# Performance work log

Hardware: AMD Instinct MI355X
Metric: run time of the kernel (lower is better)

Reference implementation:

```python
import jax, jax.numpy as jnp
import numpy as np

B, S, D, H, DQ, DV = 4, 1024, 1024, 16, 64, 64
EPS = 1e-5  # torch LayerNorm default


def setup_inputs() -> dict:
    key = jax.random.key(0)
    ks = jax.random.split(key, 6)
    x = jax.random.normal(ks[0], (B, S, D), dtype=jnp.float32)
    scale = 0.02
    return {
        "query_sequences": x,
        "key_sequences": x,   # self-attention: identical tensors
        "value_sequences": x,
        "key_value_sequence_lengths": jax.random.randint(ks[1], (B,), 512, S + 1, dtype=jnp.int32),
        "ln_gamma": jnp.ones((D,), jnp.float32),
        "ln_beta": jnp.zeros((D,), jnp.float32),
        "Wq": scale * jax.random.normal(ks[2], (D, H * DQ), jnp.float32),
        "bq": jnp.zeros((H * DQ,), jnp.float32),
        "Wk": scale * jax.random.normal(ks[3], (D, H * DQ), jnp.float32),
        "bk": jnp.zeros((H * DQ,), jnp.float32),
        "Wv": scale * jax.random.normal(ks[4], (D, H * DV), jnp.float32),
        "bv": jnp.zeros((H * DV,), jnp.float32),
    }


def _layer_norm(x, gamma, beta):
    mu = jnp.mean(x, axis=-1, keepdims=True)
    var = jnp.mean(jnp.square(x - mu), axis=-1, keepdims=True)
    return (x - mu) * jax.lax.rsqrt(var + EPS) * gamma + beta


def reference(query_sequences, key_sequences, value_sequences,
              key_value_sequence_lengths, ln_gamma, ln_beta,
              Wq, bq, Wk, bk, Wv, bv):
    # self-attention path (query/key/value sequences are identical):
    # pre-LayerNorm applied to all three, causal + pad masking, dropout=0.
    x_in = query_sequences
    xn = _layer_norm(x_in, ln_gamma, ln_beta)

    q = (xn @ Wq + bq).reshape(B, S, H, DQ).transpose(0, 2, 1, 3)  # (B,H,S,DQ)
    k = (xn @ Wk + bk).reshape(B, S, H, DQ).transpose(0, 2, 1, 3)
    v = (xn @ Wv + bv).reshape(B, S, H, DV).transpose(0, 2, 1, 3)

    scores = jnp.einsum("bhqd,bhkd->bhqk", q, k) * (1.0 / np.sqrt(DQ))

    kv_pos = jnp.arange(S)
    pad_mask = kv_pos[None, None, None, :] < key_value_sequence_lengths[:, None, None, None]
    causal = jnp.tril(jnp.ones((S, S), dtype=bool))[None, None]
    mask = pad_mask & causal
    scores = jnp.where(mask, scores, -jnp.inf)

    attn = jax.nn.softmax(scores, axis=-1)  # (B,H,S,S)

    out = jnp.einsum("bhqk,bhkd->bhqd", attn, v)          # (B,H,S,DV)
    out = out.transpose(0, 2, 1, 3).reshape(B, S, H * DV)  # (B,S,D)
    # d_model == n_heads*d_values -> cast_output is Identity; residual is plain sum
    seq = x_in + out
    return seq, attn
```

## Files before the change

### kernel.cpp

```cpp
#include <hip/hip_runtime.h>
#include <stdint.h>

#define BB 4
#define SS 1024
#define DD 1024
#define HH 16

typedef __attribute__((ext_vector_type(8))) __bf16 bf16x8;
typedef __attribute__((ext_vector_type(4))) float f32x4;

__device__ __forceinline__ unsigned short f2bf(float f) {
  union { float ff; uint32_t u; } a; a.ff = f;
  uint32_t r = a.u + 0x7fffu + ((a.u >> 16) & 1u);
  return (unsigned short)(r >> 16);
}

__device__ __forceinline__ float bf2f(unsigned short u) {
  union { uint32_t uu; float ff; } a; a.uu = ((uint32_t)u) << 16;
  return a.ff;
}

__device__ __forceinline__ f32x4 mfma16(bf16x8 a, bf16x8 b, f32x4 c) {
  return __builtin_amdgcn_mfma_f32_16x16x32_bf16(a, b, c, 0, 0, 0);
}

__device__ __forceinline__ void async16(const unsigned short* g, unsigned short* l) {
  __builtin_amdgcn_global_load_lds(
      (__attribute__((address_space(1))) void*)(g),
      (__attribute__((address_space(3))) void*)(l), 16u, 0, 0u);
}

__global__ __launch_bounds__(256) void wtrans_kernel(const float* __restrict__ Wq,
                                                     const float* __restrict__ Wk,
                                                     const float* __restrict__ Wv,
                                                     unsigned short* __restrict__ Wtq,
                                                     unsigned short* __restrict__ Wtk,
                                                     unsigned short* __restrict__ Wtv) {
  __shared__ unsigned short t[64][65];
  const int z = blockIdx.z;
  const float* W = (z == 0) ? Wq : (z == 1) ? Wk : Wv;
  unsigned short* Wt = (z == 0) ? Wtq : (z == 1) ? Wtk : Wtv;
  const int k0 = blockIdx.x * 64, n0 = blockIdx.y * 64;
  const int c = threadIdx.x & 63, r0 = threadIdx.x >> 6;
#pragma unroll
  for (int i = 0; i < 16; ++i) {
    int r = i * 4 + r0;
    t[r][c] = f2bf(W[(size_t)(k0 + r) * DD + n0 + c]);
  }
  __syncthreads();
#pragma unroll
  for (int i = 0; i < 16; ++i) {
    int n = i * 4 + r0;
    Wt[(size_t)(n0 + n) * DD + k0 + c] = t[c][n];
  }
}

__global__ __launch_bounds__(256) void ln_kernel(const float* __restrict__ X,
                                                 const float* __restrict__ gamma,
                                                 const float* __restrict__ beta,
                                                 unsigned short* __restrict__ Xn) {
  const int row = blockIdx.x;
  const int tid = threadIdx.x;
  const float* xr = X + (size_t)row * DD;
  float4 v = ((const float4*)xr)[tid];
  float s = v.x + v.y + v.z + v.w;
  float s2 = v.x * v.x + v.y * v.y + v.z * v.z + v.w * v.w;
#pragma unroll
  for (int off = 1; off < 64; off <<= 1) {
    s += __shfl_xor(s, off);
    s2 += __shfl_xor(s2, off);
  }
  __shared__ float red[8];
  const int wv = tid >> 6, lane = tid & 63;
  if (lane == 0) { red[wv] = s; red[4 + wv] = s2; }
  __syncthreads();
  s = red[0] + red[1] + red[2] + red[3];
  s2 = red[4] + red[5] + red[6] + red[7];
  const float mu = s * (1.0f / DD);
  const float rs = rsqrtf(s2 * (1.0f / DD) - mu * mu + 1e-5f);
  float4 g = ((const float4*)gamma)[tid];
  float4 bt = ((const float4*)beta)[tid];
  ushort4 o;
  o.x = f2bf((v.x - mu) * rs * g.x + bt.x);
  o.y = f2bf((v.y - mu) * rs * g.y + bt.y);
  o.z = f2bf((v.z - mu) * rs * g.z + bt.z);
  o.w = f2bf((v.w - mu) * rs * g.w + bt.w);
  ((ushort4*)(Xn + (size_t)row * DD))[tid] = o;
}

__global__ __launch_bounds__(256) void gemm_qkv_kernel(
    const unsigned short* __restrict__ Xn,
    const unsigned short* __restrict__ Wtq, const unsigned short* __restrict__ Wtk,
    const unsigned short* __restrict__ Wtv,
    const float* __restrict__ bq, const float* __restrict__ bk, const float* __restrict__ bv,
    unsigned short* __restrict__ Qb, unsigned short* __restrict__ Kb,
    unsigned short* __restrict__ Vt) {
  __shared__ __align__(16) unsigned short smem[128 * 136];
  unsigned short* sA = smem;
  unsigned short* sB = smem + 128 * 32;
  const int z = blockIdx.z;
  const unsigned short* Wt = (z == 0) ? Wtq : (z == 1) ? Wtk : Wtv;
  const float* bias = (z == 0) ? bq : (z == 1) ? bk : bv;
  const int tid = threadIdx.x;
  const int lane = tid & 63, wv = tid >> 6;
  const int quad = lane >> 4, l16 = lane & 15;
  const int m0 = blockIdx.x * 128, n0 = blockIdx.y * 128;
  const int wm = (wv & 1) * 64, wn = (wv >> 1) * 64;

  f32x4 acc[4][4];
#pragma unroll
  for (int i = 0; i < 4; ++i)
#pragma unroll
    for (int j = 0; j < 4; ++j) acc[i][j] = (f32x4){0.f, 0.f, 0.f, 0.f};

  for (int kt = 0; kt < DD; kt += 32) {
    __syncthreads();
#pragma unroll
    for (int it = 0; it < 2; ++it) {
      const int c = it * 256 + tid;
      const int row = c >> 2, kc = c & 3;
      async16(Xn + (size_t)(m0 + row) * DD + kt + kc * 8, &sA[(it * 256 + wv * 64) * 8]);
      async16(Wt + (size_t)(n0 + row) * DD + kt + kc * 8, &sB[(it * 256 + wv * 64) * 8]);
    }
    __syncthreads();
    bf16x8 af[4], bfr[4];
#pragma unroll
    for (int i = 0; i < 4; ++i) af[i] = *(const bf16x8*)&sA[(wm + i * 16 + l16) * 32 + quad * 8];
#pragma unroll
    for (int j = 0; j < 4; ++j) bfr[j] = *(const bf16x8*)&sB[(wn + j * 16 + l16) * 32 + quad * 8];
#pragma unroll
    for (int i = 0; i < 4; ++i)
#pragma unroll
      for (int j = 0; j < 4; ++j) acc[i][j] = mfma16(af[i], bfr[j], acc[i][j]);
  }

  if (z < 2) {
    __syncthreads();
    unsigned short* sC = smem;
#pragma unroll
    for (int i = 0; i < 4; ++i) {
      const int lr0 = wm + i * 16 + quad * 4;
#pragma unroll
      for (int j = 0; j < 4; ++j) {
        const int lc = wn + j * 16 + l16;
        const float bb = bias[n0 + lc];
#pragma unroll
        for (int r = 0; r < 4; ++r) sC[(lr0 + r) * 136 + lc] = f2bf(acc[i][j][r] + bb);
      }
    }
    __syncthreads();
    unsigned short* Out = (z == 0) ? Qb : Kb;
    const int rr = tid >> 4, c8 = (tid & 15) * 8;
#pragma unroll
    for (int it = 0; it < 8; ++it) {
      const int row = it * 16 + rr;
      *(uint4*)&Out[(size_t)(m0 + row) * DD + n0 + c8] = *(const uint4*)&sC[row * 136 + c8];
    }
  } else {
#pragma unroll
    for (int i = 0; i < 4; ++i) {
      const int gm0 = m0 + wm + i * 16 + quad * 4;
#pragma unroll
      for (int j = 0; j < 4; ++j) {
        const int gn = n0 + wn + j * 16 + l16;
        const float bb = bias[gn];
        const int b = gm0 >> 10, s0 = gm0 & 1023;
        const int h = gn >> 6, dv = gn & 63;
        ushort4 pk;
        pk.x = f2bf(acc[i][j][0] + bb);
        pk.y = f2bf(acc[i][j][1] + bb);
        pk.z = f2bf(acc[i][j][2] + bb);
        pk.w = f2bf(acc[i][j][3] + bb);
        *(ushort4*)&Vt[((size_t)((b * HH + h) * 64 + dv)) * SS + s0] = pk;
      }
    }
  }
}

__global__ __launch_bounds__(256) void attn_kernel(
    const unsigned short* __restrict__ Qb, const unsigned short* __restrict__ Kb,
    const unsigned short* __restrict__ Vt, const float* __restrict__ X,
    const int* __restrict__ lens, float* __restrict__ seq_out,
    float* __restrict__ attn_out) {
  __shared__ unsigned short sQV[128 * 64];
  __shared__ unsigned short sK[128 * 64];
  __shared__ unsigned short sP[4 * 32 * 128];

  const int tid = threadIdx.x;
  const int lane = tid & 63, wv = tid >> 6;
  const int quad = lane >> 4, l16 = lane & 15;
  const int h = blockIdx.y, b = blockIdx.z;
  const int qt = (b & 2) ? (7 - (int)blockIdx.x) : (int)blockIdx.x;
  const int q0 = qt * 128;
  const int len = lens[b];
  const int KE = min(q0 + 128, len);
  const int NKT = (KE + 127) >> 7;
  const float SCL = 0.1803368801111204f;

#pragma unroll
  for (int it = 0; it < 4; ++it) {
    const int c = it * 256 + tid;
    async16(Qb + (size_t)(b * SS + q0 + (c >> 3)) * DD + h * 64 + (c & 7) * 8,
            &sQV[(it * 256 + wv * 64) * 8]);
  }
  __syncthreads();

  bf16x8 qf[2][2];
#pragma unroll
  for (int i = 0; i < 2; ++i)
#pragma unroll
    for (int dd = 0; dd < 2; ++dd)
      qf[i][dd] = *(const bf16x8*)&sQV[(wv * 32 + i * 16 + l16) * 64 + dd * 32 + quad * 8];

  float lsum[2][4];
#pragma unroll
  for (int i = 0; i < 2; ++i)
#pragma unroll
    for (int r = 0; r < 4; ++r) lsum[i][r] = 0.f;

  for (int kt = 0; kt < NKT; ++kt) {
    const int k0 = kt * 128;
    __syncthreads();
#pragma unroll
    for (int it = 0; it < 4; ++it) {
      const int c = it * 256 + tid;
      async16(Kb + (size_t)(b * SS + k0 + (c >> 3)) * DD + h * 64 + (c & 7) * 8,
              &sK[(it * 256 + wv * 64) * 8]);
    }
    __syncthreads();
    const bool edge = (kt == qt) || (k0 + 128 > len);
#pragma unroll
    for (int j = 0; j < 8; ++j) {
      const bf16x8 kf0 = *(const bf16x8*)&sK[(j * 16 + l16) * 64 + quad * 8];
      const bf16x8 kf1 = *(const bf16x8*)&sK[(j * 16 + l16) * 64 + 32 + quad * 8];
      const int k = k0 + j * 16 + l16;
#pragma unroll
      for (int i = 0; i < 2; ++i) {
        f32x4 sc = (f32x4){0.f, 0.f, 0.f, 0.f};
        sc = mfma16(qf[i][0], kf0, sc);
        sc = mfma16(qf[i][1], kf1, sc);
        const int qq = q0 + wv * 32 + i * 16 + quad * 4;
#pragma unroll
        for (int r = 0; r < 4; ++r) {
          float sv = sc[r] * SCL;
          if (edge && ((k > qq + r) || (k >= len))) sv = -1e30f;
          lsum[i][r] += __builtin_amdgcn_exp2f(sv);
        }
      }
    }
  }

  float linv[2][4];
#pragma unroll
  for (int i = 0; i < 2; ++i)
#pragma unroll
    for (int r = 0; r < 4; ++r) {
      float l = lsum[i][r];
      l += __shfl_xor(l, 1);
      l += __shfl_xor(l, 2);
      l += __shfl_xor(l, 4);
      l += __shfl_xor(l, 8);
      linv[i][r] = 1.0f / l;
    }

  f32x4 oacc[2][4];
#pragma unroll
  for (int i = 0; i < 2; ++i)
#pragma unroll
    for (int jv = 0; jv < 4; ++jv) oacc[i][jv] = (f32x4){0.f, 0.f, 0.f, 0.f};

  const size_t abase = (size_t)(b * HH + h) * SS * SS;

  for (int kt = 0; kt < NKT; ++kt) {
    const int k0 = kt * 128;
    __syncthreads();
#pragma unroll
    for (int it = 0; it < 4; ++it) {
      const int c = it * 256 + tid;
      async16(Kb + (size_t)(b * SS + k0 + (c >> 3)) * DD + h * 64 + (c & 7) * 8,
              &sK[(it * 256 + wv * 64) * 8]);
      async16(Vt + ((size_t)((b * HH + h) * 64 + (c >> 4))) * SS + k0 + (c & 15) * 8,
              &sQV[(it * 256 + wv * 64) * 8]);
    }
    __syncthreads();
    const bool edge = (kt == qt) || (k0 + 128 > len);
#pragma unroll
    for (int j = 0; j < 8; ++j) {
      const bf16x8 kf0 = *(const bf16x8*)&sK[(j * 16 + l16) * 64 + quad * 8];
      const bf16x8 kf1 = *(const bf16x8*)&sK[(j * 16 + l16) * 64 + 32 + quad * 8];
      const int k = k0 + j * 16 + l16;
#pragma unroll
      for (int i = 0; i < 2; ++i) {
        f32x4 sc = (f32x4){0.f, 0.f, 0.f, 0.f};
        sc = mfma16(qf[i][0], kf0, sc);
        sc = mfma16(qf[i][1], kf1, sc);
        const int qq = q0 + wv * 32 + i * 16 + quad * 4;
        const int prow = wv * 4096 + (i * 16 + quad * 4) * 128 + j * 16 + l16;
#pragma unroll
        for (int r = 0; r < 4; ++r) {
          float sv = sc[r] * SCL;
          if (edge && ((k > qq + r) || (k >= len))) sv = -1e30f;
          const float p = __builtin_amdgcn_exp2f(sv) * linv[i][r];
          sP[prow + r * 128] = f2bf(p);
        }
      }
    }
    {
      const int r2 = lane >> 5, c32 = lane & 31;
      const size_t rowbase = abase + (size_t)(q0 + wv * 32) * SS + k0;
#pragma unroll
      for (int rr = 0; rr < 32; rr += 2) {
        const int row = rr + r2;
        ushort4 u = *(const ushort4*)&sP[wv * 4096 + row * 128 + c32 * 4];
        float4 f;
        f.x = bf2f(u.x); f.y = bf2f(u.y); f.z = bf2f(u.z); f.w = bf2f(u.w);
        *(float4*)&attn_out[rowbase + (size_t)row * SS + c32 * 4] = f;
      }
    }
#pragma unroll
    for (int kk = 0; kk < 4; ++kk) {
      bf16x8 vf[4];
#pragma unroll
      for (int jv = 0; jv < 4; ++jv)
        vf[jv] = *(const bf16x8*)&sQV[(jv * 16 + l16) * 128 + kk * 32 + quad * 8];
#pragma unroll
      for (int i = 0; i < 2; ++i) {
        const bf16x8 pf =
            *(const bf16x8*)&sP[wv * 4096 + (i * 16 + l16) * 128 + kk * 32 + quad * 8];
#pragma unroll
        for (int jv = 0; jv < 4; ++jv) oacc[i][jv] = mfma16(pf, vf[jv], oacc[i][jv]);
      }
    }
  }

  const int Z = SS - NKT * 128;
  if (Z > 0) {
    const int rr0 = tid >> 3;
    const int cf = (tid & 7) * 4;
    for (int rr = rr0; rr < 128; rr += 32) {
      float* dst = attn_out + abase + (size_t)(q0 + rr) * SS + NKT * 128 + cf;
      for (int c8 = 0; c8 < (Z >> 5); ++c8)
        *(float4*)(dst + c8 * 32) = make_float4(0.f, 0.f, 0.f, 0.f);
    }
  }

  {
    float* sPf = (float*)&sP[wv * 4096];
#pragma unroll
    for (int i = 0; i < 2; ++i)
#pragma unroll
      for (int jv = 0; jv < 4; ++jv)
#pragma unroll
        for (int r = 0; r < 4; ++r)
          sPf[(i * 16 + quad * 4 + r) * 64 + jv * 16 + l16] = oacc[i][jv][r];
    const int rr = lane >> 4, c4 = (lane & 15) * 4;
#pragma unroll
    for (int it = 0; it < 8; ++it) {
      const int lrow = it * 4 + rr;
      const size_t idx = (size_t)(b * SS + q0 + wv * 32 + lrow) * DD + h * 64 + c4;
      float4 o = *(const float4*)&sPf[lrow * 64 + c4];
      float4 x = *(const float4*)&X[idx];
      o.x += x.x; o.y += x.y; o.z += x.z; o.w += x.w;
      *(float4*)&seq_out[idx] = o;
    }
  }
}

extern "C" void kernel_launch(void* const* d_in, const int* in_sizes, int n_in,
                              void* d_out, int out_size, void* d_ws, size_t ws_size,
                              hipStream_t stream) {
  (void)in_sizes; (void)n_in; (void)out_size; (void)ws_size;
  const float* X     = (const float*)d_in[0];
  const int*   lens  = (const int*)d_in[3];
  const float* gamma = (const float*)d_in[4];
  const float* beta  = (const float*)d_in[5];
  const float* Wq    = (const float*)d_in[6];
  const float* bq    = (const float*)d_in[7];
  const float* Wk    = (const float*)d_in[8];
  const float* bk    = (const float*)d_in[9];
  const float* Wv    = (const float*)d_in[10];
  const float* bv    = (const float*)d_in[11];

  char* ws = (char*)d_ws;
  unsigned short* Xn  = (unsigned short*)(ws);
  unsigned short* Qb  = (unsigned short*)(ws + ((size_t)8  << 20));
  unsigned short* Kb  = (unsigned short*)(ws + ((size_t)16 << 20));
  unsigned short* Vt  = (unsigned short*)(ws + ((size_t)24 << 20));
  unsigned short* Wtq = (unsigned short*)(ws + ((size_t)32 << 20));
  unsigned short* Wtk = (unsigned short*)(ws + ((size_t)34 << 20));
  unsigned short* Wtv = (unsigned short*)(ws + ((size_t)36 << 20));

  float* seq_out  = (float*)d_out;
  float* attn_out = seq_out + (size_t)BB * SS * DD;

  wtrans_kernel<<<dim3(16, 16, 3), 256, 0, stream>>>(Wq, Wk, Wv, Wtq, Wtk, Wtv);
  ln_kernel<<<dim3(BB * SS), 256, 0, stream>>>(X, gamma, beta, Xn);
  gemm_qkv_kernel<<<dim3(32, 8, 3), 256, 0, stream>>>(Xn, Wtq, Wtk, Wtv, bq, bk, bv, Qb, Kb, Vt);
  attn_kernel<<<dim3(8, HH, BB), 256, 0, stream>>>(Qb, Kb, Vt, X, lens, seq_out, attn_out);
}
```

Measured before the change: 436.6 us.

## Swizzle LDS layouts, coalesce V-transpose stores, use nontemporal attn stores

Applies XOR swizzles to the Q, K, V and P shared-memory tiles in the attention kernel so that MFMA fragment reads avoid LDS bank conflicts. The V projection epilogue now transposes through shared memory and writes 16-byte coalesced rows to Vt instead of scattered 8-byte stores. The large fp32 attention-probability output and its zero padding are written with nontemporal stores to reduce cache pollution. The extra barriers and index arithmetic add some overhead.

Result: faster. 417.3 us (-4.4%).

```diff
diff --git a/kernel.cpp b/kernel.cpp
--- a/kernel.cpp
+++ b/kernel.cpp
@@ -28,6 +28,10 @@
   __builtin_amdgcn_global_load_lds(
       (__attribute__((address_space(1))) void*)(g),
       (__attribute__((address_space(3))) void*)(l), 16u, 0, 0u);
+}
+
+__device__ __forceinline__ void nt_store4(float* p, f32x4 v) {
+  __builtin_nontemporal_store(v, (f32x4*)p);
 }
 
 __global__ __launch_bounds__(256) void wtrans_kernel(const float* __restrict__ Wq,
@@ -134,8 +138,8 @@
       for (int j = 0; j < 4; ++j) acc[i][j] = mfma16(af[i], bfr[j], acc[i][j]);
   }
 
+  __syncthreads();
   if (z < 2) {
-    __syncthreads();
     unsigned short* sC = smem;
 #pragma unroll
     for (int i = 0; i < 4; ++i) {
@@ -157,22 +161,28 @@
       *(uint4*)&Out[(size_t)(m0 + row) * DD + n0 + c8] = *(const uint4*)&sC[row * 136 + c8];
     }
   } else {
+    unsigned short* sC = smem;
 #pragma unroll
     for (int i = 0; i < 4; ++i) {
-      const int gm0 = m0 + wm + i * 16 + quad * 4;
+      const int lr0 = wm + i * 16 + quad * 4;
 #pragma unroll
       for (int j = 0; j < 4; ++j) {
-        const int gn = n0 + wn + j * 16 + l16;
-        const float bb = bias[gn];
-        const int b = gm0 >> 10, s0 = gm0 & 1023;
-        const int h = gn >> 6, dv = gn & 63;
-        ushort4 pk;
-        pk.x = f2bf(acc[i][j][0] + bb);
-        pk.y = f2bf(acc[i][j][1] + bb);
-        pk.z = f2bf(acc[i][j][2] + bb);
-        pk.w = f2bf(acc[i][j][3] + bb);
-        *(ushort4*)&Vt[((size_t)((b * HH + h) * 64 + dv)) * SS + s0] = pk;
-      }
+        const int lc = wn + j * 16 + l16;
+        const float bb = bias[n0 + lc];
+#pragma unroll
+        for (int r = 0; r < 4; ++r) sC[lc * 136 + lr0 + r] = f2bf(acc[i][j][r] + bb);
+      }
+    }
+    __syncthreads();
+    const int b = m0 >> 10, s0 = m0 & 1023;
+    const int rr = tid >> 4, c8 = (tid & 15) * 8;
+#pragma unroll
+    for (int it = 0; it < 8; ++it) {
+      const int row = it * 16 + rr;
+      const int n = n0 + row;
+      unsigned short* dst =
+          &Vt[((size_t)((b * HH + (n >> 6)) * 64 + (n & 63))) * SS + s0 + c8];
+      *(uint4*)dst = *(const uint4*)&sC[row * 136 + c8];
     }
   }
 }
@@ -196,11 +206,13 @@
   const int KE = min(q0 + 128, len);
   const int NKT = (KE + 127) >> 7;
   const float SCL = 0.1803368801111204f;
+  const int s7 = l16 & 7;
 
 #pragma unroll
   for (int it = 0; it < 4; ++it) {
     const int c = it * 256 + tid;
-    async16(Qb + (size_t)(b * SS + q0 + (c >> 3)) * DD + h * 64 + (c & 7) * 8,
+    const int row = c >> 3, ch = (c & 7) ^ (row & 7);
+    async16(Qb + (size_t)(b * SS + q0 + row) * DD + h * 64 + ch * 8,
             &sQV[(it * 256 + wv * 64) * 8]);
   }
   __syncthreads();
@@ -210,7 +222,8 @@
   for (int i = 0; i < 2; ++i)
 #pragma unroll
     for (int dd = 0; dd < 2; ++dd)
-      qf[i][dd] = *(const bf16x8*)&sQV[(wv * 32 + i * 16 + l16) * 64 + dd * 32 + quad * 8];
+      qf[i][dd] = *(const bf16x8*)
+          &sQV[(wv * 32 + i * 16 + l16) * 64 + ((dd * 4 + quad) ^ s7) * 8];
 
   float lsum[2][4];
 #pragma unroll
@@ -224,15 +237,16 @@
 #pragma unroll
     for (int it = 0; it < 4; ++it) {
       const int c = it * 256 + tid;
-      async16(Kb + (size_t)(b * SS + k0 + (c >> 3)) * DD + h * 64 + (c & 7) * 8,
+      const int row = c >> 3, ch = (c & 7) ^ (row & 7);
+      async16(Kb + (size_t)(b * SS + k0 + row) * DD + h * 64 + ch * 8,
               &sK[(it * 256 + wv * 64) * 8]);
     }
     __syncthreads();
     const bool edge = (kt == qt) || (k0 + 128 > len);
 #pragma unroll
     for (int j = 0; j < 8; ++j) {
-      const bf16x8 kf0 = *(const bf16x8*)&sK[(j * 16 + l16) * 64 + quad * 8];
-      const bf16x8 kf1 = *(const bf16x8*)&sK[(j * 16 + l16) * 64 + 32 + quad * 8];
+      const bf16x8 kf0 = *(const bf16x8*)&sK[(j * 16 + l16) * 64 + ((0 + quad) ^ s7) * 8];
+      const bf16x8 kf1 = *(const bf16x8*)&sK[(j * 16 + l16) * 64 + ((4 + quad) ^ s7) * 8];
       const int k = k0 + j * 16 + l16;
 #pragma unroll
       for (int i = 0; i < 2; ++i) {
@@ -277,17 +291,19 @@
 #pragma unroll
     for (int it = 0; it < 4; ++it) {
       const int c = it * 256 + tid;
-      async16(Kb + (size_t)(b * SS + k0 + (c >> 3)) * DD + h * 64 + (c & 7) * 8,
+      const int krow = c >> 3, kch = (c & 7) ^ (krow & 7);
+      async16(Kb + (size_t)(b * SS + k0 + krow) * DD + h * 64 + kch * 8,
               &sK[(it * 256 + wv * 64) * 8]);
-      async16(Vt + ((size_t)((b * HH + h) * 64 + (c >> 4))) * SS + k0 + (c & 15) * 8,
+      const int vrow = c >> 4, vch = (c & 15) ^ (vrow & 15);
+      async16(Vt + ((size_t)((b * HH + h) * 64 + vrow)) * SS + k0 + vch * 8,
               &sQV[(it * 256 + wv * 64) * 8]);
     }
     __syncthreads();
     const bool edge = (kt == qt) || (k0 + 128 > len);
 #pragma unroll
     for (int j = 0; j < 8; ++j) {
-      const bf16x8 kf0 = *(const bf16x8*)&sK[(j * 16 + l16) * 64 + quad * 8];
-      const bf16x8 kf1 = *(const bf16x8*)&sK[(j * 16 + l16) * 64 + 32 + quad * 8];
+      const bf16x8 kf0 = *(const bf16x8*)&sK[(j * 16 + l16) * 64 + ((0 + quad) ^ s7) * 8];
+      const bf16x8 kf1 = *(const bf16x8*)&sK[(j * 16 + l16) * 64 + ((4 + quad) ^ s7) * 8];
       const int k = k0 + j * 16 + l16;
 #pragma unroll
       for (int i = 0; i < 2; ++i) {
@@ -295,26 +311,27 @@
         sc = mfma16(qf[i][0], kf0, sc);
         sc = mfma16(qf[i][1], kf1, sc);
         const int qq = q0 + wv * 32 + i * 16 + quad * 4;
-        const int prow = wv * 4096 + (i * 16 + quad * 4) * 128 + j * 16 + l16;
 #pragma unroll
         for (int r = 0; r < 4; ++r) {
           float sv = sc[r] * SCL;
           if (edge && ((k > qq + r) || (k >= len))) sv = -1e30f;
           const float p = __builtin_amdgcn_exp2f(sv) * linv[i][r];
-          sP[prow + r * 128] = f2bf(p);
+          const int prow = i * 16 + quad * 4 + r;
+          const int pch = (2 * j + (l16 >> 3)) ^ (prow & 15);
+          sP[wv * 4096 + prow * 128 + pch * 8 + (l16 & 7)] = f2bf(p);
         }
       }
     }
     {
       const int r2 = lane >> 5, c32 = lane & 31;
-      const size_t rowbase = abase + (size_t)(q0 + wv * 32) * SS + k0;
 #pragma unroll
       for (int rr = 0; rr < 32; rr += 2) {
         const int row = rr + r2;
-        ushort4 u = *(const ushort4*)&sP[wv * 4096 + row * 128 + c32 * 4];
-        float4 f;
-        f.x = bf2f(u.x); f.y = bf2f(u.y); f.z = bf2f(u.z); f.w = bf2f(u.w);
-        *(float4*)&attn_out[rowbase + (size_t)row * SS + c32 * 4] = f;
+        const int ch = (c32 >> 1) ^ (row & 15);
+        ushort4 u = *(const ushort4*)&sP[wv * 4096 + row * 128 + ch * 8 + (c32 & 1) * 4];
+        f32x4 f;
+        f[0] = bf2f(u.x); f[1] = bf2f(u.y); f[2] = bf2f(u.z); f[3] = bf2f(u.w);
+        nt_store4(&attn_out[abase + (size_t)(q0 + wv * 32 + row) * SS + k0 + c32 * 4], f);
       }
     }
 #pragma unroll
@@ -322,11 +339,12 @@
       bf16x8 vf[4];
 #pragma unroll
       for (int jv = 0; jv < 4; ++jv)
-        vf[jv] = *(const bf16x8*)&sQV[(jv * 16 + l16) * 128 + kk * 32 + quad * 8];
+        vf[jv] = *(const bf16x8*)
+            &sQV[(jv * 16 + l16) * 128 + (((kk * 4 + quad) ^ l16) & 15) * 8];
 #pragma unroll
       for (int i = 0; i < 2; ++i) {
-        const bf16x8 pf =
-            *(const bf16x8*)&sP[wv * 4096 + (i * 16 + l16) * 128 + kk * 32 + quad * 8];
+        const bf16x8 pf = *(const bf16x8*)
+            &sP[wv * 4096 + (i * 16 + l16) * 128 + ((kk * 4 + quad) ^ l16) * 8];
 #pragma unroll
         for (int jv = 0; jv < 4; ++jv) oacc[i][jv] = mfma16(pf, vf[jv], oacc[i][jv]);
       }
@@ -337,13 +355,14 @@
   if (Z > 0) {
     const int rr0 = tid >> 3;
     const int cf = (tid & 7) * 4;
+    const f32x4 zz = (f32x4){0.f, 0.f, 0.f, 0.f};
     for (int rr = rr0; rr < 128; rr += 32) {
       float* dst = attn_out + abase + (size_t)(q0 + rr) * SS + NKT * 128 + cf;
-      for (int c8 = 0; c8 < (Z >> 5); ++c8)
-        *(float4*)(dst + c8 * 32) = make_float4(0.f, 0.f, 0.f, 0.f);
-    }
-  }
-
+      for (int c8 = 0; c8 < (Z >> 5); ++c8) nt_store4(dst + c8 * 32, zz);
+    }
+  }
+
+  __syncthreads();
   {
     float* sPf = (float*)&sP[wv * 4096];
 #pragma unroll
```
